# Kernel optimization log

Measured on AMD Instinct MI355X. Metric: run time of the kernel, lower is better.

The kernel has to match this reference:

```python
import jax, jax.numpy as jnp
import numpy as np

TOP_K = 2
NUM_EXPERTS = 8
LB_COEFF = 0.01


def setup_inputs() -> dict:
    key = jax.random.key(0)
    ks = jax.random.split(key, 5)
    B, S, D, F, E = 4, 2048, 1024, 4096, NUM_EXPERTS
    s_in = 0.02
    return {
        "x": jax.random.normal(ks[0], (B, S, D), jnp.float32),
        "gate_w": jax.random.normal(ks[1], (D, E), jnp.float32) * s_in,
        "gate_b": jnp.zeros((E,), jnp.float32),
        "fc1_w": jax.random.normal(ks[2], (E, D, 2 * F), jnp.float32) * s_in,
        "fc1_b": jnp.zeros((E, 2 * F), jnp.float32),
        "fc2_w": jax.random.normal(ks[3], (E, F, D), jnp.float32) * s_in,
        "fc2_b": jnp.zeros((E, D), jnp.float32),
    }


def reference(x, gate_w, gate_b, fc1_w, fc1_b, fc2_w, fc2_b):
    B, S, D = x.shape
    E = gate_w.shape[1]
    xt = x.reshape(-1, D)                      # [T, D]
    T = xt.shape[0]

    gate_logits = xt @ gate_w + gate_b        # [T, E]
    gate_probs = jax.nn.softmax(gate_logits, axis=-1)
    top_w, top_i = jax.lax.top_k(gate_probs, TOP_K)      # [T, K]
    w_norm = top_w / (top_w.sum(-1, keepdims=True) + 1e-6)

    rows = jnp.arange(T)[:, None]
    # per-token per-expert combine weight (0 if expert not in top-k)
    combine = jnp.zeros((T, E), xt.dtype).at[rows, top_i].add(w_norm)  # [T, E]

    out = jnp.zeros_like(xt)
    for e in range(E):  # fixed small expert loop; each is a dense GEMM
        h = xt @ fc1_w[e] + fc1_b[e]                      # [T, 2F]
        a, g = jnp.split(h, 2, axis=-1)
        act = a * jax.nn.gelu(g, approximate=False)       # SwiGLU (exact gelu, torch default)
        y = act @ fc2_w[e] + fc2_b[e]                     # [T, D]
        out = out + combine[:, e:e + 1] * y

    chosen_mask = jnp.zeros((T, E), gate_probs.dtype).at[rows, top_i].set(1.0)
    frac = chosen_mask.mean(0)
    mean_probs = gate_probs.mean(0)
    lb_loss = LB_COEFF * E * jnp.sum(frac * mean_probs)

    return out.reshape(B, S, D), lb_loss
```

## Files before the change

### kernel.cpp

```cpp
#include <hip/hip_runtime.h>
#include <hip/hip_bf16.h>
#include <stdint.h>

typedef __attribute__((ext_vector_type(4))) float f32x4;
typedef __attribute__((ext_vector_type(16))) float f32x16;
typedef __attribute__((ext_vector_type(8))) __bf16 bf16x8;
typedef __attribute__((ext_vector_type(4))) unsigned short u16x4;
typedef unsigned short u16;

#define NTOK 8192
#define DDIM 1024
#define FDIM 4096
#define NEXP 8
#define NT1 144

#define WS_XB    0ull
#define WS_W1T   (16777216ull)
#define WS_W2T   (WS_W1T + 134217728ull)
#define WS_ACT   (WS_W2T + 67108864ull)
#define WS_LIST  (WS_ACT + 142606336ull)
#define WS_PAIRW (WS_LIST + 262144ull)
#define WS_CNT   (WS_PAIRW + 262144ull)
#define WS_SUMP  (WS_CNT + 32ull)
#define WS_PAD   (WS_SUMP + 32ull)
#define WS_OFF   (WS_PAD + 32ull)
#define WS_T1E   (WS_OFF + 32ull)
#define WS_T1R   (WS_T1E + 1024ull)

static __device__ __forceinline__ u16 bf16rne(float f) {
  union { float f; uint32_t u; } c; c.f = f;
  return (u16)((c.u + 0x7FFFu + ((c.u >> 16) & 1u)) >> 16);
}

static __device__ __forceinline__ void load_lds16(const void* g, void* l) {
  __builtin_amdgcn_global_load_lds((const __attribute__((address_space(1))) void*)g,
                                   (__attribute__((address_space(3))) void*)l, 16, 0, 0);
}

__global__ __launch_bounds__(256) void gate_kernel(
    const float* __restrict__ x, const float* __restrict__ gw,
    const float* __restrict__ gb, u16* __restrict__ xb,
    int* __restrict__ cnt, float* __restrict__ sump,
    int* __restrict__ list, float* __restrict__ pairw) {
  const int tid = threadIdx.x;
  const int lane = tid & 63;
  const int wv = tid >> 6;
  const int t = blockIdx.x * 4 + wv;

  __shared__ float sp[8];
  if (tid < 8) sp[tid] = 0.f;
  __syncthreads();

  float acc[8] = {0.f,0.f,0.f,0.f,0.f,0.f,0.f,0.f};
  const float4* x4 = (const float4*)x + (size_t)t * 256;
  u16x4* xb4 = (u16x4*)xb + (size_t)t * 256;
  #pragma unroll
  for (int it = 0; it < 4; ++it) {
    const float4 xv = x4[it * 64 + lane];
    u16x4 bv;
    bv[0] = bf16rne(xv.x); bv[1] = bf16rne(xv.y);
    bv[2] = bf16rne(xv.z); bv[3] = bf16rne(xv.w);
    xb4[it * 64 + lane] = bv;
    const int d0 = (it * 64 + lane) * 4;
    #pragma unroll
    for (int j = 0; j < 4; ++j) {
      const float xs = (j == 0) ? xv.x : ((j == 1) ? xv.y : ((j == 2) ? xv.z : xv.w));
      const float* g = gw + (size_t)(d0 + j) * 8;
      #pragma unroll
      for (int e2 = 0; e2 < 8; ++e2) acc[e2] += xs * g[e2];
    }
  }
  #pragma unroll
  for (int e2 = 0; e2 < 8; ++e2) {
    float v = acc[e2];
    v += __shfl_xor(v, 1);  v += __shfl_xor(v, 2);  v += __shfl_xor(v, 4);
    v += __shfl_xor(v, 8);  v += __shfl_xor(v, 16); v += __shfl_xor(v, 32);
    acc[e2] = v;
  }
  float p[8]; float mx = -1e30f;
  #pragma unroll
  for (int e2 = 0; e2 < 8; ++e2) { p[e2] = acc[e2] + gb[e2]; mx = fmaxf(mx, p[e2]); }
  float s = 0.f;
  #pragma unroll
  for (int e2 = 0; e2 < 8; ++e2) { p[e2] = expf(p[e2] - mx); s += p[e2]; }
  const float inv = 1.f / s;
  #pragma unroll
  for (int e2 = 0; e2 < 8; ++e2) p[e2] *= inv;

  if (lane == 0) {
    int i1 = 0; float v1 = p[0];
    #pragma unroll
    for (int e2 = 1; e2 < 8; ++e2) if (p[e2] > v1) { v1 = p[e2]; i1 = e2; }
    int i2 = 0; float v2 = -1.f;
    #pragma unroll
    for (int e2 = 0; e2 < 8; ++e2) if (e2 != i1 && p[e2] > v2) { v2 = p[e2]; i2 = e2; }
    const float den = v1 + v2 + 1e-6f;
    const int p1 = atomicAdd(&cnt[i1], 1);
    list[i1 * NTOK + p1] = t; pairw[i1 * NTOK + p1] = v1 / den;
    const int p2 = atomicAdd(&cnt[i2], 1);
    list[i2 * NTOK + p2] = t; pairw[i2 * NTOK + p2] = v2 / den;
    #pragma unroll
    for (int e2 = 0; e2 < 8; ++e2) atomicAdd(&sp[e2], p[e2]);
  }
  __syncthreads();
  if (tid < 8) atomicAdd(&sump[tid], sp[tid]);
}

__global__ __launch_bounds__(256) void conv_transpose(
    const float* __restrict__ in, u16* __restrict__ out, int R, int C) {
  __shared__ float tile[64][65];
  const int e = blockIdx.z;
  const float* pin = in + (size_t)e * R * C;
  u16* pout = out + (size_t)e * R * C;
  const int tx = threadIdx.x & 15;
  const int ty = threadIdx.x >> 4;
  const int c0 = blockIdx.x * 64;
  const int r0 = blockIdx.y * 64;
  #pragma unroll
  for (int i = 0; i < 4; ++i) {
    const int r = ty + i * 16;
    const float4 v = *(const float4*)(pin + (size_t)(r0 + r) * C + c0 + tx * 4);
    tile[r][tx * 4 + 0] = v.x;
    tile[r][tx * 4 + 1] = v.y;
    tile[r][tx * 4 + 2] = v.z;
    tile[r][tx * 4 + 3] = v.w;
  }
  __syncthreads();
  #pragma unroll
  for (int i = 0; i < 4; ++i) {
    const int c = ty + i * 16;
    u16x4 o;
    o[0] = bf16rne(tile[tx * 4 + 0][c]);
    o[1] = bf16rne(tile[tx * 4 + 1][c]);
    o[2] = bf16rne(tile[tx * 4 + 2][c]);
    o[3] = bf16rne(tile[tx * 4 + 3][c]);
    *(u16x4*)(pout + (size_t)(c0 + c) * R + r0 + tx * 4) = o;
  }
}

__global__ void route_finalize(const int* __restrict__ cnt, const float* __restrict__ sump,
                               int* __restrict__ padc, int* __restrict__ offs,
                               int* __restrict__ list, float* __restrict__ pairw,
                               int* __restrict__ t1e, int* __restrict__ t1r,
                               float* __restrict__ lb_out) {
  __shared__ int s_c[8], s_p[8];
  const int tid = threadIdx.x;
  if (tid == 0) {
    int o = 0; float lb = 0.f;
    for (int e = 0; e < 8; ++e) {
      const int c = cnt[e];
      const int pc = (c + 127) & ~127;
      s_c[e] = c; s_p[e] = pc;
      padc[e] = pc; offs[e] = o; o += pc;
      lb += ((float)c / 8192.f) * (sump[e] / 8192.f);
    }
    lb_out[0] = 0.01f * 8.f * lb;
    int n1 = 0;
    for (int e = 0; e < 8; ++e)
      for (int r = 0; r < s_p[e]; r += 128) { t1e[n1] = e; t1r[n1] = r; ++n1; }
    for (; n1 < NT1; ++n1) { t1e[n1] = -1; t1r[n1] = 0; }
  }
  __syncthreads();
  for (int e = 0; e < 8; ++e)
    for (int pq = s_c[e] + tid; pq < s_p[e]; pq += blockDim.x) {
      list[e * NTOK + pq] = 0; pairw[e * NTOK + pq] = 0.f;
    }
}

__global__ __launch_bounds__(256) void gemm1_kernel(
    const u16* __restrict__ xb, const u16* __restrict__ w1t,
    const float* __restrict__ b1, const int* __restrict__ list,
    const int* __restrict__ offs,
    const int* __restrict__ t1e, const int* __restrict__ t1r,
    u16* __restrict__ act) {
  const int tt = blockIdx.y;
  const int e = t1e[tt];
  if (e < 0) return;
  const int row0 = t1r[tt];
  const int j = blockIdx.x;
  const int off_e = offs[e];

  __shared__ u16 lds[16384];

  const int tid = threadIdx.x;
  const int lane = tid & 63;
  const int wv = tid >> 6;
  const int wr = wv >> 1, wc = wv & 1;
  const int l31 = lane & 31, s5 = lane >> 5;

  const int rt = tid >> 2;
  const int ce = ((tid & 3) ^ ((rt >> 1) & 3)) * 8;
  const int tok0 = list[e * NTOK + row0 + rt];
  const int tok1 = list[e * NTOK + row0 + rt + 64];
  const u16* srcA0 = xb + (size_t)tok0 * DDIM + ce;
  const u16* srcA1 = xb + (size_t)tok1 * DDIM + ce;
  const int rB1 = rt + 64;
  const int gn0 = j * 64 + ((rt >> 6) & 1) * 32 + (rt & 31) + ((rt >> 5) & 1) * FDIM;
  const int gn1 = j * 64 + ((rB1 >> 6) & 1) * 32 + (rB1 & 31) + ((rB1 >> 5) & 1) * FDIM;
  const u16* srcB0 = w1t + ((size_t)e * 2 * FDIM + gn0) * DDIM + ce;
  const u16* srcB1 = w1t + ((size_t)e * 2 * FDIM + gn1) * DDIM + ce;

  const int xsw = (l31 >> 1) & 3;
  const int kel0 = (s5 ^ xsw) * 8;
  const int aB0 = (wr * 64 + l31) * 32 + kel0;  const int aB1 = aB0 ^ 16;
  const int bB0 = (wc * 64 + l31) * 32 + kel0;  const int bB1 = bB0 ^ 16;

  f32x16 acc[2][2];
  #pragma unroll
  for (int m = 0; m < 2; ++m)
    #pragma unroll
    for (int n = 0; n < 2; ++n)
      #pragma unroll
      for (int i = 0; i < 16; ++i) acc[m][n][i] = 0.f;

  #define STAGE1(buf, kt) do { \
    u16* _dA = &lds[(buf) * 4096 + wv * 512]; \
    u16* _dB = &lds[8192 + (buf) * 4096 + wv * 512]; \
    load_lds16(srcA0 + (kt) * 32, _dA); \
    load_lds16(srcA1 + (kt) * 32, _dA + 2048); \
    load_lds16(srcB0 + (kt) * 32, _dB); \
    load_lds16(srcB1 + (kt) * 32, _dB + 2048); \
  } while (0)

  STAGE1(0, 0);
  for (int kt = 0; kt < DDIM / 32; ++kt) {
    const int cur = kt & 1;
    __syncthreads();
    if (kt + 1 < DDIM / 32) STAGE1(cur ^ 1, kt + 1);
    const int bA = cur * 4096;
    const int bB = 8192 + cur * 4096;
    bf16x8 a0[2], a1[2], Bh0[2], Bh1[2];
    #pragma unroll
    for (int m = 0; m < 2; ++m) {
      a0[m] = *(const bf16x8*)&lds[bA + aB0 + m * 1024];
      a1[m] = *(const bf16x8*)&lds[bA + aB1 + m * 1024];
    }
    #pragma unroll
    for (int n = 0; n < 2; ++n) {
      Bh0[n] = *(const bf16x8*)&lds[bB + bB0 + n * 1024];
      Bh1[n] = *(const bf16x8*)&lds[bB + bB1 + n * 1024];
    }
    #pragma unroll
    for (int m = 0; m < 2; ++m)
      #pragma unroll
      for (int n = 0; n < 2; ++n) {
        acc[m][n] = __builtin_amdgcn_mfma_f32_32x32x16_bf16(a0[m], Bh0[n], acc[m][n], 0, 0, 0);
        acc[m][n] = __builtin_amdgcn_mfma_f32_32x32x16_bf16(a1[m], Bh1[n], acc[m][n], 0, 0, 0);
      }
  }
  #undef STAGE1

  const size_t actrow0 = (size_t)(off_e + row0);
  const int col = j * 64 + wc * 32 + l31;
  const float ba = b1[e * (2 * FDIM) + col];
  const float bg = b1[e * (2 * FDIM) + FDIM + col];
  #pragma unroll
  for (int m = 0; m < 2; ++m) {
    #pragma unroll
    for (int r = 0; r < 16; ++r) {
      const int row = wr * 64 + m * 32 + (r & 3) + 8 * (r >> 2) + 4 * s5;
      const float a = acc[m][0][r] + ba;
      const float g = acc[m][1][r] + bg;
      const float u2 = 1.5957691216057308f * (g + 0.044715f * g * g * g);
      const float sg = 1.f / (1.f + __expf(-u2));
      act[(actrow0 + row) * FDIM + col] = bf16rne(a * g * sg);
    }
  }
}

__global__ __launch_bounds__(256) void gemm2_kernel(
    const u16* __restrict__ act, const u16* __restrict__ w2t,
    const float* __restrict__ b2, const int* __restrict__ list,
    const float* __restrict__ pairw, const int* __restrict__ offs,
    const int* __restrict__ t1e, const int* __restrict__ t1r,
    float* __restrict__ out) {
  const int bid = blockIdx.x;
  const int r8 = bid & 7;
  const int q = bid >> 3;
  const int jt = q & 7;
  const int tt = (q >> 3) * 8 + r8;
  const int e = t1e[tt];
  if (e < 0) return;
  const int row0 = t1r[tt];
  const int off_e = offs[e];

  __shared__ u16 lds[16384];

  const int tid = threadIdx.x;
  const int lane = tid & 63;
  const int wv = tid >> 6;
  const int wr = wv >> 1, wc = wv & 1;
  const int l31 = lane & 31, s5 = lane >> 5;

  const int rt = tid >> 2;
  const int ce = ((tid & 3) ^ ((rt >> 1) & 3)) * 8;
  const u16* srcA0 = act + (size_t)(off_e + row0 + rt) * FDIM + ce;
  const u16* srcA1 = act + (size_t)(off_e + row0 + rt + 64) * FDIM + ce;
  const u16* srcB0 = w2t + ((size_t)e * DDIM + jt * 128 + rt) * FDIM + ce;
  const u16* srcB1 = w2t + ((size_t)e * DDIM + jt * 128 + rt + 64) * FDIM + ce;

  const int xsw = (l31 >> 1) & 3;
  const int kel0 = (s5 ^ xsw) * 8;
  const int aB0 = (wr * 64 + l31) * 32 + kel0;  const int aB1 = aB0 ^ 16;
  const int bB0 = (wc * 64 + l31) * 32 + kel0;  const int bB1 = bB0 ^ 16;

  f32x16 acc[2][2];
  #pragma unroll
  for (int m = 0; m < 2; ++m)
    #pragma unroll
    for (int n = 0; n < 2; ++n)
      #pragma unroll
      for (int i = 0; i < 16; ++i) acc[m][n][i] = 0.f;

  #define STAGE2(buf, kt) do { \
    u16* _dA = &lds[(buf) * 4096 + wv * 512]; \
    u16* _dB = &lds[8192 + (buf) * 4096 + wv * 512]; \
    load_lds16(srcA0 + (kt) * 32, _dA); \
    load_lds16(srcA1 + (kt) * 32, _dA + 2048); \
    load_lds16(srcB0 + (kt) * 32, _dB); \
    load_lds16(srcB1 + (kt) * 32, _dB + 2048); \
  } while (0)

  STAGE2(0, 0);
  for (int kt = 0; kt < FDIM / 32; ++kt) {
    const int cur = kt & 1;
    __syncthreads();
    if (kt + 1 < FDIM / 32) STAGE2(cur ^ 1, kt + 1);
    const int bA = cur * 4096;
    const int bB = 8192 + cur * 4096;
    bf16x8 a0[2], a1[2], Bh0[2], Bh1[2];
    #pragma unroll
    for (int m = 0; m < 2; ++m) {
      a0[m] = *(const bf16x8*)&lds[bA + aB0 + m * 1024];
      a1[m] = *(const bf16x8*)&lds[bA + aB1 + m * 1024];
    }
    #pragma unroll
    for (int n = 0; n < 2; ++n) {
      Bh0[n] = *(const bf16x8*)&lds[bB + bB0 + n * 1024];
      Bh1[n] = *(const bf16x8*)&lds[bB + bB1 + n * 1024];
    }
    #pragma unroll
    for (int m = 0; m < 2; ++m)
      #pragma unroll
      for (int n = 0; n < 2; ++n) {
        acc[m][n] = __builtin_amdgcn_mfma_f32_32x32x16_bf16(a0[m], Bh0[n], acc[m][n], 0, 0, 0);
        acc[m][n] = __builtin_amdgcn_mfma_f32_32x32x16_bf16(a1[m], Bh1[n], acc[m][n], 0, 0, 0);
      }
  }
  #undef STAGE2

  #pragma unroll
  for (int m = 0; m < 2; ++m) {
    #pragma unroll
    for (int r = 0; r < 16; ++r) {
      const int row = wr * 64 + m * 32 + (r & 3) + 8 * (r >> 2) + 4 * s5;
      const int pos = row0 + row;
      const int tok = list[e * NTOK + pos];
      const float pw = pairw[e * NTOK + pos];
      if (pw != 0.f) {
        #pragma unroll
        for (int n = 0; n < 2; ++n) {
          const int col = jt * 128 + wc * 64 + n * 32 + l31;
          const float v = (acc[m][n][r] + b2[e * DDIM + col]) * pw;
          atomicAdd(&out[(size_t)tok * DDIM + col], v);
        }
      }
    }
  }
}

extern "C" void kernel_launch(void* const* d_in, const int* in_sizes, int n_in,
                              void* d_out, int out_size, void* d_ws, size_t ws_size,
                              hipStream_t stream) {
  const float* x   = (const float*)d_in[0];
  const float* gw  = (const float*)d_in[1];
  const float* gb  = (const float*)d_in[2];
  const float* f1w = (const float*)d_in[3];
  const float* f1b = (const float*)d_in[4];
  const float* f2w = (const float*)d_in[5];
  const float* f2b = (const float*)d_in[6];
  float* out = (float*)d_out;
  char* ws = (char*)d_ws;

  u16*   xb    = (u16*)(ws + WS_XB);
  u16*   w1t   = (u16*)(ws + WS_W1T);
  u16*   w2t   = (u16*)(ws + WS_W2T);
  u16*   act   = (u16*)(ws + WS_ACT);
  int*   list  = (int*)(ws + WS_LIST);
  float* pairw = (float*)(ws + WS_PAIRW);
  int*   cnt   = (int*)(ws + WS_CNT);
  float* sump  = (float*)(ws + WS_SUMP);
  int*   padc  = (int*)(ws + WS_PAD);
  int*   offs  = (int*)(ws + WS_OFF);
  int*   t1e   = (int*)(ws + WS_T1E);
  int*   t1r   = (int*)(ws + WS_T1R);

  (void)hipMemsetAsync(d_out, 0, (size_t)out_size * sizeof(float), stream);
  (void)hipMemsetAsync(ws + WS_CNT, 0, 64, stream);

  gate_kernel<<<NTOK / 4, 256, 0, stream>>>(x, gw, gb, xb, cnt, sump, list, pairw);
  conv_transpose<<<dim3(8192 / 64, 1024 / 64, 8), 256, 0, stream>>>(f1w, w1t, 1024, 8192);
  conv_transpose<<<dim3(1024 / 64, 4096 / 64, 8), 256, 0, stream>>>(f2w, w2t, 4096, 1024);
  route_finalize<<<1, 256, 0, stream>>>(cnt, sump, padc, offs, list, pairw,
                                        t1e, t1r, out + 8388608);
  gemm1_kernel<<<dim3(64, NT1), 256, 0, stream>>>(xb, w1t, f1b, list, offs, t1e, t1r, act);
  gemm2_kernel<<<NT1 * 8, 256, 0, stream>>>(act, w2t, f2b, list, pairw, offs, t1e, t1r, out);
}
```

Baseline: 996.4 us.

## Replace atomic scatter with per-slot output buffer plus gather, simplify LDS staging layout

gemm2 now writes weighted expert outputs non-atomically into a per-slot fp32 buffer that reuses the w1t workspace region, and a new gather kernel sums each token's two slot rows into the output. This removes the output memset and the float atomics, at the cost of an extra write and read of the slot buffer. Separately, both GEMMs drop the XOR-swizzled LDS staging: each lane now loads one row's 16-byte chunks laid out directly in MFMA fragment order, which simplifies indexing but changes the global-load access pattern and may affect coalescing. Padded slots with zero pair weight are left unwritten in y; gather only reads real slots, so this appears safe.

```diff
diff --git a/kernel.cpp b/kernel.cpp
--- a/kernel.cpp
+++ b/kernel.cpp
@@ -26,6 +26,8 @@
 #define WS_OFF   (WS_PAD + 32ull)
 #define WS_T1E   (WS_OFF + 32ull)
 #define WS_T1R   (WS_T1E + 1024ull)
+#define WS_SE    (WS_T1R + 1024ull)
+#define WS_SP    (WS_SE + 65536ull)
 
 static __device__ __forceinline__ u16 bf16rne(float f) {
   union { float f; uint32_t u; } c; c.f = f;
@@ -41,7 +43,8 @@
     const float* __restrict__ x, const float* __restrict__ gw,
     const float* __restrict__ gb, u16* __restrict__ xb,
     int* __restrict__ cnt, float* __restrict__ sump,
-    int* __restrict__ list, float* __restrict__ pairw) {
+    int* __restrict__ list, float* __restrict__ pairw,
+    int* __restrict__ slotE, int* __restrict__ slotP) {
   const int tid = threadIdx.x;
   const int lane = tid & 63;
   const int wv = tid >> 6;
@@ -97,8 +100,10 @@
     const float den = v1 + v2 + 1e-6f;
     const int p1 = atomicAdd(&cnt[i1], 1);
     list[i1 * NTOK + p1] = t; pairw[i1 * NTOK + p1] = v1 / den;
+    slotE[2 * t] = i1; slotP[2 * t] = p1;
     const int p2 = atomicAdd(&cnt[i2], 1);
     list[i2 * NTOK + p2] = t; pairw[i2 * NTOK + p2] = v2 / den;
+    slotE[2 * t + 1] = i2; slotP[2 * t + 1] = p2;
     #pragma unroll
     for (int e2 = 0; e2 < 8; ++e2) atomicAdd(&sp[e2], p[e2]);
   }
@@ -188,22 +193,11 @@
   const int wr = wv >> 1, wc = wv & 1;
   const int l31 = lane & 31, s5 = lane >> 5;
 
-  const int rt = tid >> 2;
-  const int ce = ((tid & 3) ^ ((rt >> 1) & 3)) * 8;
-  const int tok0 = list[e * NTOK + row0 + rt];
-  const int tok1 = list[e * NTOK + row0 + rt + 64];
-  const u16* srcA0 = xb + (size_t)tok0 * DDIM + ce;
-  const u16* srcA1 = xb + (size_t)tok1 * DDIM + ce;
-  const int rB1 = rt + 64;
-  const int gn0 = j * 64 + ((rt >> 6) & 1) * 32 + (rt & 31) + ((rt >> 5) & 1) * FDIM;
-  const int gn1 = j * 64 + ((rB1 >> 6) & 1) * 32 + (rB1 & 31) + ((rB1 >> 5) & 1) * FDIM;
-  const u16* srcB0 = w1t + ((size_t)e * 2 * FDIM + gn0) * DDIM + ce;
-  const u16* srcB1 = w1t + ((size_t)e * 2 * FDIM + gn1) * DDIM + ce;
-
-  const int xsw = (l31 >> 1) & 3;
-  const int kel0 = (s5 ^ xsw) * 8;
-  const int aB0 = (wr * 64 + l31) * 32 + kel0;  const int aB1 = aB0 ^ 16;
-  const int bB0 = (wc * 64 + l31) * 32 + kel0;  const int bB1 = bB0 ^ 16;
+  const int ra = wv * 32 + l31;
+  const int tok = list[e * NTOK + row0 + ra];
+  const u16* srcA = xb + (size_t)tok * DDIM + s5 * 8;
+  const int gn = j * 64 + ((ra >> 6) & 1) * 32 + (ra & 31) + ((ra >> 5) & 1) * FDIM;
+  const u16* srcB = w1t + ((size_t)e * 2 * FDIM + gn) * DDIM + s5 * 8;
 
   f32x16 acc[2][2];
   #pragma unroll
@@ -214,52 +208,54 @@
       for (int i = 0; i < 16; ++i) acc[m][n][i] = 0.f;
 
   #define STAGE1(buf, kt) do { \
-    u16* _dA = &lds[(buf) * 4096 + wv * 512]; \
-    u16* _dB = &lds[8192 + (buf) * 4096 + wv * 512]; \
-    load_lds16(srcA0 + (kt) * 32, _dA); \
-    load_lds16(srcA1 + (kt) * 32, _dA + 2048); \
-    load_lds16(srcB0 + (kt) * 32, _dB); \
-    load_lds16(srcB1 + (kt) * 32, _dB + 2048); \
+    u16* _dA = &lds[(buf) * 4096 + wv * 1024]; \
+    u16* _dB = &lds[8192 + (buf) * 4096 + wv * 1024]; \
+    load_lds16(srcA + (kt) * 32, _dA); \
+    load_lds16(srcA + (kt) * 32 + 16, _dA + 512); \
+    load_lds16(srcB + (kt) * 32, _dB); \
+    load_lds16(srcB + (kt) * 32 + 16, _dB + 512); \
   } while (0)
+
+  const int aOff = wr * 2048 + lane * 8;
+  const int bOff = 8192 + wc * 2048 + lane * 8;
 
   STAGE1(0, 0);
   for (int kt = 0; kt < DDIM / 32; ++kt) {
     const int cur = kt & 1;
     __syncthreads();
     if (kt + 1 < DDIM / 32) STAGE1(cur ^ 1, kt + 1);
-    const int bA = cur * 4096;
-    const int bB = 8192 + cur * 4096;
-    bf16x8 a0[2], a1[2], Bh0[2], Bh1[2];
+    const int ba = cur * 4096;
+    bf16x8 aF[2][2], bF[2][2];
     #pragma unroll
     for (int m = 0; m < 2; ++m) {
-      a0[m] = *(const bf16x8*)&lds[bA + aB0 + m * 1024];
-      a1[m] = *(const bf16x8*)&lds[bA + aB1 + m * 1024];
+      aF[m][0] = *(const bf16x8*)&lds[ba + aOff + m * 1024];
+      aF[m][1] = *(const bf16x8*)&lds[ba + aOff + m * 1024 + 512];
     }
     #pragma unroll
     for (int n = 0; n < 2; ++n) {
-      Bh0[n] = *(const bf16x8*)&lds[bB + bB0 + n * 1024];
-      Bh1[n] = *(const bf16x8*)&lds[bB + bB1 + n * 1024];
+      bF[n][0] = *(const bf16x8*)&lds[ba + bOff + n * 1024];
+      bF[n][1] = *(const bf16x8*)&lds[ba + bOff + n * 1024 + 512];
     }
     #pragma unroll
     for (int m = 0; m < 2; ++m)
       #pragma unroll
       for (int n = 0; n < 2; ++n) {
-        acc[m][n] = __builtin_amdgcn_mfma_f32_32x32x16_bf16(a0[m], Bh0[n], acc[m][n], 0, 0, 0);
-        acc[m][n] = __builtin_amdgcn_mfma_f32_32x32x16_bf16(a1[m], Bh1[n], acc[m][n], 0, 0, 0);
+        acc[m][n] = __builtin_amdgcn_mfma_f32_32x32x16_bf16(aF[m][0], bF[n][0], acc[m][n], 0, 0, 0);
+        acc[m][n] = __builtin_amdgcn_mfma_f32_32x32x16_bf16(aF[m][1], bF[n][1], acc[m][n], 0, 0, 0);
       }
   }
   #undef STAGE1
 
   const size_t actrow0 = (size_t)(off_e + row0);
   const int col = j * 64 + wc * 32 + l31;
-  const float ba = b1[e * (2 * FDIM) + col];
+  const float ba2 = b1[e * (2 * FDIM) + col];
   const float bg = b1[e * (2 * FDIM) + FDIM + col];
   #pragma unroll
   for (int m = 0; m < 2; ++m) {
     #pragma unroll
     for (int r = 0; r < 16; ++r) {
       const int row = wr * 64 + m * 32 + (r & 3) + 8 * (r >> 2) + 4 * s5;
-      const float a = acc[m][0][r] + ba;
+      const float a = acc[m][0][r] + ba2;
       const float g = acc[m][1][r] + bg;
       const float u2 = 1.5957691216057308f * (g + 0.044715f * g * g * g);
       const float sg = 1.f / (1.f + __expf(-u2));
@@ -270,10 +266,10 @@
 
 __global__ __launch_bounds__(256) void gemm2_kernel(
     const u16* __restrict__ act, const u16* __restrict__ w2t,
-    const float* __restrict__ b2, const int* __restrict__ list,
-    const float* __restrict__ pairw, const int* __restrict__ offs,
+    const float* __restrict__ b2, const float* __restrict__ pairw,
+    const int* __restrict__ offs,
     const int* __restrict__ t1e, const int* __restrict__ t1r,
-    float* __restrict__ out) {
+    float* __restrict__ y) {
   const int bid = blockIdx.x;
   const int r8 = bid & 7;
   const int q = bid >> 3;
@@ -292,17 +288,9 @@
   const int wr = wv >> 1, wc = wv & 1;
   const int l31 = lane & 31, s5 = lane >> 5;
 
-  const int rt = tid >> 2;
-  const int ce = ((tid & 3) ^ ((rt >> 1) & 3)) * 8;
-  const u16* srcA0 = act + (size_t)(off_e + row0 + rt) * FDIM + ce;
-  const u16* srcA1 = act + (size_t)(off_e + row0 + rt + 64) * FDIM + ce;
-  const u16* srcB0 = w2t + ((size_t)e * DDIM + jt * 128 + rt) * FDIM + ce;
-  const u16* srcB1 = w2t + ((size_t)e * DDIM + jt * 128 + rt + 64) * FDIM + ce;
-
-  const int xsw = (l31 >> 1) & 3;
-  const int kel0 = (s5 ^ xsw) * 8;
-  const int aB0 = (wr * 64 + l31) * 32 + kel0;  const int aB1 = aB0 ^ 16;
-  const int bB0 = (wc * 64 + l31) * 32 + kel0;  const int bB1 = bB0 ^ 16;
+  const int ra = wv * 32 + l31;
+  const u16* srcA = act + (size_t)(off_e + row0 + ra) * FDIM + s5 * 8;
+  const u16* srcB = w2t + ((size_t)e * DDIM + jt * 128 + ra) * FDIM + s5 * 8;
 
   f32x16 acc[2][2];
   #pragma unroll
@@ -313,38 +301,40 @@
       for (int i = 0; i < 16; ++i) acc[m][n][i] = 0.f;
 
   #define STAGE2(buf, kt) do { \
-    u16* _dA = &lds[(buf) * 4096 + wv * 512]; \
-    u16* _dB = &lds[8192 + (buf) * 4096 + wv * 512]; \
-    load_lds16(srcA0 + (kt) * 32, _dA); \
-    load_lds16(srcA1 + (kt) * 32, _dA + 2048); \
-    load_lds16(srcB0 + (kt) * 32, _dB); \
-    load_lds16(srcB1 + (kt) * 32, _dB + 2048); \
+    u16* _dA = &lds[(buf) * 4096 + wv * 1024]; \
+    u16* _dB = &lds[8192 + (buf) * 4096 + wv * 1024]; \
+    load_lds16(srcA + (kt) * 32, _dA); \
+    load_lds16(srcA + (kt) * 32 + 16, _dA + 512); \
+    load_lds16(srcB + (kt) * 32, _dB); \
+    load_lds16(srcB + (kt) * 32 + 16, _dB + 512); \
   } while (0)
+
+  const int aOff = wr * 2048 + lane * 8;
+  const int bOff = 8192 + wc * 2048 + lane * 8;
 
   STAGE2(0, 0);
   for (int kt = 0; kt < FDIM / 32; ++kt) {
     const int cur = kt & 1;
     __syncthreads();
     if (kt + 1 < FDIM / 32) STAGE2(cur ^ 1, kt + 1);
-    const int bA = cur * 4096;
-    const int bB = 8192 + cur * 4096;
-    bf16x8 a0[2], a1[2], Bh0[2], Bh1[2];
+    const int ba = cur * 4096;
+    bf16x8 aF[2][2], bF[2][2];
     #pragma unroll
     for (int m = 0; m < 2; ++m) {
-      a0[m] = *(const bf16x8*)&lds[bA + aB0 + m * 1024];
-      a1[m] = *(const bf16x8*)&lds[bA + aB1 + m * 1024];
+      aF[m][0] = *(const bf16x8*)&lds[ba + aOff + m * 1024];
+      aF[m][1] = *(const bf16x8*)&lds[ba + aOff + m * 1024 + 512];
     }
     #pragma unroll
     for (int n = 0; n < 2; ++n) {
-      Bh0[n] = *(const bf16x8*)&lds[bB + bB0 + n * 1024];
-      Bh1[n] = *(const bf16x8*)&lds[bB + bB1 + n * 1024];
+      bF[n][0] = *(const bf16x8*)&lds[ba + bOff + n * 1024];
+      bF[n][1] = *(const bf16x8*)&lds[ba + bOff + n * 1024 + 512];
     }
     #pragma unroll
     for (int m = 0; m < 2; ++m)
       #pragma unroll
       for (int n = 0; n < 2; ++n) {
-        acc[m][n] = __builtin_amdgcn_mfma_f32_32x32x16_bf16(a0[m], Bh0[n], acc[m][n], 0, 0, 0);
-        acc[m][n] = __builtin_amdgcn_mfma_f32_32x32x16_bf16(a1[m], Bh1[n], acc[m][n], 0, 0, 0);
+        acc[m][n] = __builtin_amdgcn_mfma_f32_32x32x16_bf16(aF[m][0], bF[n][0], acc[m][n], 0, 0, 0);
+        acc[m][n] = __builtin_amdgcn_mfma_f32_32x32x16_bf16(aF[m][1], bF[n][1], acc[m][n], 0, 0, 0);
       }
   }
   #undef STAGE2
@@ -355,17 +345,36 @@
     for (int r = 0; r < 16; ++r) {
       const int row = wr * 64 + m * 32 + (r & 3) + 8 * (r >> 2) + 4 * s5;
       const int pos = row0 + row;
-      const int tok = list[e * NTOK + pos];
       const float pw = pairw[e * NTOK + pos];
       if (pw != 0.f) {
+        float* yr = y + (size_t)(off_e + pos) * DDIM;
         #pragma unroll
         for (int n = 0; n < 2; ++n) {
           const int col = jt * 128 + wc * 64 + n * 32 + l31;
-          const float v = (acc[m][n][r] + b2[e * DDIM + col]) * pw;
-          atomicAdd(&out[(size_t)tok * DDIM + col], v);
+          yr[col] = (acc[m][n][r] + b2[e * DDIM + col]) * pw;
         }
       }
     }
+  }
+}
+
+__global__ __launch_bounds__(256) void gather_kernel(
+    const float* __restrict__ y, const int* __restrict__ slotE,
+    const int* __restrict__ slotP, const int* __restrict__ offs,
+    float* __restrict__ out) {
+  const int t = blockIdx.x * 4 + (threadIdx.x >> 6);
+  const int lane = threadIdx.x & 63;
+  const int r1 = offs[slotE[2 * t]] + slotP[2 * t];
+  const int r2 = offs[slotE[2 * t + 1]] + slotP[2 * t + 1];
+  const float4* y1 = (const float4*)(y + (size_t)r1 * DDIM);
+  const float4* y2 = (const float4*)(y + (size_t)r2 * DDIM);
+  float4* o4 = (float4*)(out + (size_t)t * DDIM);
+  #pragma unroll
+  for (int i = 0; i < 4; ++i) {
+    const float4 a = y1[i * 64 + lane];
+    const float4 b = y2[i * 64 + lane];
+    float4 r; r.x = a.x + b.x; r.y = a.y + b.y; r.z = a.z + b.z; r.w = a.w + b.w;
+    o4[i * 64 + lane] = r;
   }
 }
 
@@ -384,6 +393,7 @@
 
   u16*   xb    = (u16*)(ws + WS_XB);
   u16*   w1t   = (u16*)(ws + WS_W1T);
+  float* y     = (float*)(ws + WS_W1T);
   u16*   w2t   = (u16*)(ws + WS_W2T);
   u16*   act   = (u16*)(ws + WS_ACT);
   int*   list  = (int*)(ws + WS_LIST);
@@ -394,15 +404,17 @@
   int*   offs  = (int*)(ws + WS_OFF);
   int*   t1e   = (int*)(ws + WS_T1E);
   int*   t1r   = (int*)(ws + WS_T1R);
-
-  (void)hipMemsetAsync(d_out, 0, (size_t)out_size * sizeof(float), stream);
+  int*   slotE = (int*)(ws + WS_SE);
+  int*   slotP = (int*)(ws + WS_SP);
+
   (void)hipMemsetAsync(ws + WS_CNT, 0, 64, stream);
 
-  gate_kernel<<<NTOK / 4, 256, 0, stream>>>(x, gw, gb, xb, cnt, sump, list, pairw);
+  gate_kernel<<<NTOK / 4, 256, 0, stream>>>(x, gw, gb, xb, cnt, sump, list, pairw, slotE, slotP);
   conv_transpose<<<dim3(8192 / 64, 1024 / 64, 8), 256, 0, stream>>>(f1w, w1t, 1024, 8192);
   conv_transpose<<<dim3(1024 / 64, 4096 / 64, 8), 256, 0, stream>>>(f2w, w2t, 4096, 1024);
   route_finalize<<<1, 256, 0, stream>>>(cnt, sump, padc, offs, list, pairw,
                                         t1e, t1r, out + 8388608);
   gemm1_kernel<<<dim3(64, NT1), 256, 0, stream>>>(xb, w1t, f1b, list, offs, t1e, t1r, act);
-  gemm2_kernel<<<NT1 * 8, 256, 0, stream>>>(act, w2t, f2b, list, pairw, offs, t1e, t1r, out);
-}
+  gemm2_kernel<<<NT1 * 8, 256, 0, stream>>>(act, w2t, f2b, pairw, offs, t1e, t1r, y);
+  gather_kernel<<<NTOK / 4, 256, 0, stream>>>(y, slotE, slotP, offs, out);
+}
```

After: 1.241 ms. 24.6% more time.

## Replace atomic scatter in expert GEMM2 with staged writes plus token gather

Applied to the files above, without the earlier changes.

GEMM2 now writes each weighted expert row into a contiguous staging buffer (reusing the fc1 weight workspace) instead of issuing float atomicAdds into the output. A new gather kernel sums each token's two expert rows using per-token slot indices recorded by the gate kernel. This drops the output memset and the atomic traffic, but adds an extra write and read of the staging buffer and one more kernel launch.

```diff
diff --git a/kernel.cpp b/kernel.cpp
--- a/kernel.cpp
+++ b/kernel.cpp
@@ -26,6 +26,8 @@
 #define WS_OFF   (WS_PAD + 32ull)
 #define WS_T1E   (WS_OFF + 32ull)
 #define WS_T1R   (WS_T1E + 1024ull)
+#define WS_SE    (WS_T1R + 1024ull)
+#define WS_SP    (WS_SE + 65536ull)
 
 static __device__ __forceinline__ u16 bf16rne(float f) {
   union { float f; uint32_t u; } c; c.f = f;
@@ -41,7 +43,8 @@
     const float* __restrict__ x, const float* __restrict__ gw,
     const float* __restrict__ gb, u16* __restrict__ xb,
     int* __restrict__ cnt, float* __restrict__ sump,
-    int* __restrict__ list, float* __restrict__ pairw) {
+    int* __restrict__ list, float* __restrict__ pairw,
+    int* __restrict__ slotE, int* __restrict__ slotP) {
   const int tid = threadIdx.x;
   const int lane = tid & 63;
   const int wv = tid >> 6;
@@ -97,8 +100,10 @@
     const float den = v1 + v2 + 1e-6f;
     const int p1 = atomicAdd(&cnt[i1], 1);
     list[i1 * NTOK + p1] = t; pairw[i1 * NTOK + p1] = v1 / den;
+    slotE[2 * t] = i1; slotP[2 * t] = p1;
     const int p2 = atomicAdd(&cnt[i2], 1);
     list[i2 * NTOK + p2] = t; pairw[i2 * NTOK + p2] = v2 / den;
+    slotE[2 * t + 1] = i2; slotP[2 * t + 1] = p2;
     #pragma unroll
     for (int e2 = 0; e2 < 8; ++e2) atomicAdd(&sp[e2], p[e2]);
   }
@@ -270,10 +275,10 @@
 
 __global__ __launch_bounds__(256) void gemm2_kernel(
     const u16* __restrict__ act, const u16* __restrict__ w2t,
-    const float* __restrict__ b2, const int* __restrict__ list,
-    const float* __restrict__ pairw, const int* __restrict__ offs,
+    const float* __restrict__ b2, const float* __restrict__ pairw,
+    const int* __restrict__ offs,
     const int* __restrict__ t1e, const int* __restrict__ t1r,
-    float* __restrict__ out) {
+    float* __restrict__ y) {
   const int bid = blockIdx.x;
   const int r8 = bid & 7;
   const int q = bid >> 3;
@@ -355,17 +360,36 @@
     for (int r = 0; r < 16; ++r) {
       const int row = wr * 64 + m * 32 + (r & 3) + 8 * (r >> 2) + 4 * s5;
       const int pos = row0 + row;
-      const int tok = list[e * NTOK + pos];
       const float pw = pairw[e * NTOK + pos];
       if (pw != 0.f) {
+        float* yr = y + (size_t)(off_e + pos) * DDIM;
         #pragma unroll
         for (int n = 0; n < 2; ++n) {
           const int col = jt * 128 + wc * 64 + n * 32 + l31;
-          const float v = (acc[m][n][r] + b2[e * DDIM + col]) * pw;
-          atomicAdd(&out[(size_t)tok * DDIM + col], v);
+          yr[col] = (acc[m][n][r] + b2[e * DDIM + col]) * pw;
         }
       }
     }
+  }
+}
+
+__global__ __launch_bounds__(256) void gather_kernel(
+    const float* __restrict__ y, const int* __restrict__ slotE,
+    const int* __restrict__ slotP, const int* __restrict__ offs,
+    float* __restrict__ out) {
+  const int t = blockIdx.x * 4 + (threadIdx.x >> 6);
+  const int lane = threadIdx.x & 63;
+  const int r1 = offs[slotE[2 * t]] + slotP[2 * t];
+  const int r2 = offs[slotE[2 * t + 1]] + slotP[2 * t + 1];
+  const float4* y1 = (const float4*)(y + (size_t)r1 * DDIM);
+  const float4* y2 = (const float4*)(y + (size_t)r2 * DDIM);
+  float4* o4 = (float4*)(out + (size_t)t * DDIM);
+  #pragma unroll
+  for (int i = 0; i < 4; ++i) {
+    const float4 a = y1[i * 64 + lane];
+    const float4 b = y2[i * 64 + lane];
+    float4 r; r.x = a.x + b.x; r.y = a.y + b.y; r.z = a.z + b.z; r.w = a.w + b.w;
+    o4[i * 64 + lane] = r;
   }
 }
 
@@ -384,6 +408,7 @@
 
   u16*   xb    = (u16*)(ws + WS_XB);
   u16*   w1t   = (u16*)(ws + WS_W1T);
+  float* y     = (float*)(ws + WS_W1T);
   u16*   w2t   = (u16*)(ws + WS_W2T);
   u16*   act   = (u16*)(ws + WS_ACT);
   int*   list  = (int*)(ws + WS_LIST);
@@ -394,15 +419,17 @@
   int*   offs  = (int*)(ws + WS_OFF);
   int*   t1e   = (int*)(ws + WS_T1E);
   int*   t1r   = (int*)(ws + WS_T1R);
-
-  (void)hipMemsetAsync(d_out, 0, (size_t)out_size * sizeof(float), stream);
+  int*   slotE = (int*)(ws + WS_SE);
+  int*   slotP = (int*)(ws + WS_SP);
+
   (void)hipMemsetAsync(ws + WS_CNT, 0, 64, stream);
 
-  gate_kernel<<<NTOK / 4, 256, 0, stream>>>(x, gw, gb, xb, cnt, sump, list, pairw);
+  gate_kernel<<<NTOK / 4, 256, 0, stream>>>(x, gw, gb, xb, cnt, sump, list, pairw, slotE, slotP);
   conv_transpose<<<dim3(8192 / 64, 1024 / 64, 8), 256, 0, stream>>>(f1w, w1t, 1024, 8192);
   conv_transpose<<<dim3(1024 / 64, 4096 / 64, 8), 256, 0, stream>>>(f2w, w2t, 4096, 1024);
   route_finalize<<<1, 256, 0, stream>>>(cnt, sump, padc, offs, list, pairw,
                                         t1e, t1r, out + 8388608);
   gemm1_kernel<<<dim3(64, NT1), 256, 0, stream>>>(xb, w1t, f1b, list, offs, t1e, t1r, act);
-  gemm2_kernel<<<NT1 * 8, 256, 0, stream>>>(act, w2t, f2b, list, pairw, offs, t1e, t1r, out);
-}
+  gemm2_kernel<<<NT1 * 8, 256, 0, stream>>>(act, w2t, f2b, pairw, offs, t1e, t1r, y);
+  gather_kernel<<<NTOK / 4, 256, 0, stream>>>(y, slotE, slotP, offs, out);
+}
```

After: 951.9 us. -4.5%, faster.
